# Optimization experiments

Measured on AMD Instinct MI355X. Metric: run time of the kernel, lower is better.

Reference implementation:

```python
import jax, jax.numpy as jnp
import numpy as np
from jax import lax

BLANK = 0


def _rnnt_loss_single(lp, tgt, T_n, U_n):
    """lp: (T, U+1, C) log-probs; tgt: (U,) int32; T_n, U_n: scalar lengths.
    Returns the negative log-likelihood via the alpha forward recursion."""
    T, U1, C = lp.shape
    U = U1 - 1
    blank_lp = lp[:, :, BLANK]                                   # (T, U+1)
    # emit_lp[t, u] = lp[t, u, tgt[u]]
    emit_lp = jnp.take_along_axis(
        lp[:, :U, :], tgt[None, :, None].astype(jnp.int32), axis=2
    )[..., 0]                                                    # (T, U)

    # alpha[0, u] = sum_{v<u} emit_lp[0, v]
    row0 = jnp.concatenate(
        [jnp.zeros((1,), lp.dtype), jnp.cumsum(emit_lp[0])]
    )                                                            # (U+1,)

    def outer(prev_row, xs):
        b_prev, e_row = xs                   # blank_lp[t-1], emit_lp[t]
        c = prev_row + b_prev                # come-from-below (blank) term

        def inner(carry, xs2):
            c_u, e_um1 = xs2
            val = jnp.logaddexp(c_u, carry + e_um1)
            return val, val

        _, rest = lax.scan(inner, c[0], (c[1:], e_row))
        row = jnp.concatenate([c[:1], rest])
        return row, row

    _, rows = lax.scan(outer, row0, (blank_lp[:-1], emit_lp[1:]))
    alpha = jnp.concatenate([row0[None, :], rows], axis=0)       # (T, U+1)

    # log P = alpha[T_n-1, U_n] + log p(blank | T_n-1, U_n)
    ll = alpha[T_n - 1, U_n] + blank_lp[T_n - 1, U_n]
    return -ll


def setup_inputs() -> dict:
    key = jax.random.key(0)
    k1, k2 = jax.random.split(key)
    N, T, U, C = 8, 256, 128, 512
    activations = jax.random.normal(k1, (N, T, U + 1, C), dtype=jnp.float32)
    targets = jax.random.randint(k2, (N, U), 1, C, dtype=jnp.int32)
    activation_lengths = jnp.full((N,), T, dtype=jnp.int32)
    target_lengths = jnp.full((N,), U, dtype=jnp.int32)
    return {
        "activations": activations,
        "targets": targets,
        "activation_lengths": activation_lengths,
        "target_lengths": target_lengths,
    }


def reference(activations, targets, activation_lengths, target_lengths):
    lp = jax.nn.log_softmax(activations, axis=-1)                # (N,T,U+1,C)
    losses = jax.vmap(_rnnt_loss_single)(
        lp, targets, activation_lengths, target_lengths
    )                                                            # (N,)
    return jnp.mean(losses)  # reduction='mean'
```

## Files before the change

### kernel.cpp

```cpp
#include <hip/hip_runtime.h>


#define C_CLASSES 512

__device__ __forceinline__ float wave_max(float v) {
    for (int off = 32; off > 0; off >>= 1)
        v = fmaxf(v, __shfl_xor(v, off, 64));
    return v;
}
__device__ __forceinline__ float wave_sum(float v) {
    for (int off = 32; off > 0; off >>= 1)
        v += __shfl_xor(v, off, 64);
    return v;
}
__device__ __forceinline__ float lae(float a, float b) {
    float m = fmaxf(a, b);
    float t = __expf(-fabsf(a - b));
    return m + __logf(1.0f + t);
}

__global__ __launch_bounds__(256) void k1_lse(
    const float* __restrict__ act, const int* __restrict__ tgt,
    float* __restrict__ blankD, float* __restrict__ emitD,
    int N, int T, int U, int rowsTotal, int dstride, int sampleStride)
{
    const int wave = threadIdx.x >> 6;
    const int lane = threadIdx.x & 63;
    const int r = blockIdx.x * 4 + wave;
    if (r >= rowsTotal) return;

    const int U1 = U + 1;
    const int TU1 = T * U1;
    const int n = r / TU1;
    const int rem = r - n * TU1;
    const int t = rem / U1;
    const int u = rem - t * U1;

    const float4* rp = (const float4*)(act + (size_t)r * C_CLASSES);
    const float4 a = rp[lane];
    const float4 b = rp[64 + lane];

    float m = fmaxf(fmaxf(a.x, a.y), fmaxf(a.z, a.w));
    m = fmaxf(m, fmaxf(fmaxf(b.x, b.y), fmaxf(b.z, b.w)));
    m = wave_max(m);
    float s = __expf(a.x - m) + __expf(a.y - m) + __expf(a.z - m) + __expf(a.w - m)
            + __expf(b.x - m) + __expf(b.y - m) + __expf(b.z - m) + __expf(b.w - m);
    s = wave_sum(s);
    const float lse = m + __logf(s);

    const int d = t + u + 1;
    const size_t base = (size_t)n * sampleStride + (size_t)d * dstride;
    if (lane == 0)
        blankD[base + u] = a.x - lse;
    if (u < U) {
        const int k = tgt[n * U + u];
        const int owner = (k < 256) ? (k >> 2) : ((k - 256) >> 2);
        if (lane == owner) {
            const float4 src = (k < 256) ? a : b;
            const int kk = k & 3;
            const float v = (kk & 2) ? ((kk & 1) ? src.w : src.z)
                                     : ((kk & 1) ? src.y : src.x);
            emitD[base + (u + 1)] = v - lse;
        }
    }
}

__global__ __launch_bounds__(64) void k2_alpha(
    const float* __restrict__ blankD, const float* __restrict__ emitD,
    const int* __restrict__ alen, const int* __restrict__ tlen,
    float* __restrict__ losses, int dstride, int sampleStride)
{
    const int n = blockIdx.x;
    const int l = threadIdx.x;
    const int Tn = alen[n];
    const int Un = tlen[n];
    const int Tn1 = Tn - 1;
    const int Dend = Tn1 + Un;

    const float* __restrict__ bS = blankD + (size_t)n * sampleStride;
    const float* __restrict__ eS = emitD  + (size_t)n * sampleStride;

    const float NEG = -1e30f;
    const int u0 = 2 * l, u1 = 2 * l + 1;

    float p0 = (l == 0) ? 0.0f : NEG;
    float p1 = NEG, p2 = NEG;

    float2 bA, eA, bB, eB;
    float b2A, e2A, b2B, e2B;
#define LDIAG(d, bb, ee, b2, e2)                                   \
    {                                                              \
        const float* brow = bS + (size_t)(d) * dstride;            \
        const float* erow = eS + (size_t)(d) * dstride;            \
        bb = *(const float2*)(brow + u0);                          \
        ee = *(const float2*)(erow + u0);                          \
        b2 = brow[128]; e2 = erow[128];                            \
    }

    LDIAG(1, bA, eA, b2A, e2A);
    LDIAG(2, bB, eB, b2B, e2B);

    for (int d = 1; d <= Dend; ++d) {
        const float2 bb = bA, ee = eA;
        const float b2 = b2A, e2 = e2A;
        bA = bB; eA = eB; b2A = b2B; e2A = e2B;
        int dpf = d + 2; if (dpf > Dend + 1) dpf = Dend + 1;
        LDIAG(dpf, bB, eB, b2B, e2B);

        const float pm1 = __shfl_up(p1, 1, 64);

        const int t0 = d - u0, t1 = d - u1, t2 = d - 128;
        const bool v0 = (t0 >= 0) && (t0 <= Tn1) && (u0 <= Un);
        const bool v1 = (t1 >= 0) && (t1 <= Tn1) && (u1 <= Un);
        const bool v2 = (t2 >= 0) && (t2 <= Tn1) && (128 <= Un);

        const float a0 = (v0 && t0 >= 1) ? p0 + bb.x : NEG;
        const float g0 = (v0 && u0 >= 1) ? pm1 + ee.x : NEG;
        const float a1 = (v1 && t1 >= 1) ? p1 + bb.y : NEG;
        const float g1 = v1 ? p0 + ee.y : NEG;
        const float a2 = (v2 && t2 >= 1) ? p2 + b2 : NEG;
        const float g2 = v2 ? p1 + e2 : NEG;

        const float n0 = lae(a0, g0);
        const float n1 = lae(a1, g1);
        const float n2 = lae(a2, g2);
        p0 = n0; p1 = n1; p2 = n2;
    }
#undef LDIAG

    const float fb = bS[(size_t)(Dend + 1) * dstride + Un];
    if (u0 == Un) losses[n] = -(p0 + fb);
    if (u1 == Un) losses[n] = -(p1 + fb);
    if (l == 63 && Un == 128) losses[n] = -(p2 + fb);
}

__global__ void k3_mean(const float* __restrict__ losses, float* __restrict__ out, int N)
{
    if (threadIdx.x == 0) {
        float s = 0.0f;
        for (int i = 0; i < N; ++i) s += losses[i];
        out[0] = s / (float)N;
    }
}

extern "C" void kernel_launch(void* const* d_in, const int* in_sizes, int n_in,
                              void* d_out, int out_size, void* d_ws, size_t ws_size,
                              hipStream_t stream)
{
    const float* act  = (const float*)d_in[0];
    const int*   tgt  = (const int*)d_in[1];
    const int*   alen = (const int*)d_in[2];
    const int*   tlen = (const int*)d_in[3];

    const int N  = in_sizes[2];
    const int U  = in_sizes[1] / N;
    const int U1 = U + 1;
    const int T  = (int)((long long)in_sizes[0] / ((long long)N * U1 * C_CLASSES));

    const int rows = N * T * U1;
    const int dstride = U1 + 1;
    const int sampleStride = (T + U + 1) * dstride;

    float* ws = (float*)d_ws;
    float* blankD = ws;
    float* emitD  = ws + (size_t)N * sampleStride;
    float* losses = emitD + (size_t)N * sampleStride;

    k1_lse<<<(rows + 3) / 4, 256, 0, stream>>>(act, tgt, blankD, emitD,
                                               N, T, U, rows, dstride, sampleStride);
    k2_alpha<<<N, 64, 0, stream>>>(blankD, emitD, alen, tlen, losses,
                                   dstride, sampleStride);
    k3_mean<<<1, 64, 0, stream>>>(losses, (float*)d_out, N);
}
```

Baseline: 897.3 us.

## Deepen alpha prefetch, use nontemporal loads, fuse mean via atomics

```diff
diff --git a/kernel.cpp b/kernel.cpp
--- a/kernel.cpp
+++ b/kernel.cpp
@@ -2,6 +2,8 @@
 
 
 #define C_CLASSES 512
+
+typedef float v4f __attribute__((ext_vector_type(4)));
 
 __device__ __forceinline__ float wave_max(float v) {
     for (int off = 32; off > 0; off >>= 1)
@@ -22,8 +24,11 @@
 __global__ __launch_bounds__(256) void k1_lse(
     const float* __restrict__ act, const int* __restrict__ tgt,
     float* __restrict__ blankD, float* __restrict__ emitD,
+    float* __restrict__ accum, int* __restrict__ count,
     int N, int T, int U, int rowsTotal, int dstride, int sampleStride)
 {
+    if (blockIdx.x == 0 && threadIdx.x == 0) { accum[0] = 0.0f; count[0] = 0; }
+
     const int wave = threadIdx.x >> 6;
     const int lane = threadIdx.x & 63;
     const int r = blockIdx.x * 4 + wave;
@@ -36,9 +41,9 @@
     const int t = rem / U1;
     const int u = rem - t * U1;
 
-    const float4* rp = (const float4*)(act + (size_t)r * C_CLASSES);
-    const float4 a = rp[lane];
-    const float4 b = rp[64 + lane];
+    const v4f* rp = (const v4f*)(act + (size_t)r * C_CLASSES);
+    const v4f a = __builtin_nontemporal_load(rp + lane);
+    const v4f b = __builtin_nontemporal_load(rp + 64 + lane);
 
     float m = fmaxf(fmaxf(a.x, a.y), fmaxf(a.z, a.w));
     m = fmaxf(m, fmaxf(fmaxf(b.x, b.y), fmaxf(b.z, b.w)));
@@ -56,7 +61,7 @@
         const int k = tgt[n * U + u];
         const int owner = (k < 256) ? (k >> 2) : ((k - 256) >> 2);
         if (lane == owner) {
-            const float4 src = (k < 256) ? a : b;
+            const v4f src = (k < 256) ? a : b;
             const int kk = k & 3;
             const float v = (kk & 2) ? ((kk & 1) ? src.w : src.z)
                                      : ((kk & 1) ? src.y : src.x);
@@ -65,10 +70,12 @@
     }
 }
 
+#define PF 8
 __global__ __launch_bounds__(64) void k2_alpha(
     const float* __restrict__ blankD, const float* __restrict__ emitD,
     const int* __restrict__ alen, const int* __restrict__ tlen,
-    float* __restrict__ losses, int dstride, int sampleStride)
+    float* __restrict__ accum, int* __restrict__ count,
+    float* __restrict__ out, int N, int dstride, int sampleStride)
 {
     const int n = blockIdx.x;
     const int l = threadIdx.x;
@@ -86,8 +93,8 @@
     float p0 = (l == 0) ? 0.0f : NEG;
     float p1 = NEG, p2 = NEG;
 
-    float2 bA, eA, bB, eB;
-    float b2A, e2A, b2B, e2B;
+    float2 bQ[PF], eQ[PF];
+    float b2Q[PF], e2Q[PF];
 #define LDIAG(d, bb, ee, b2, e2)                                   \
     {                                                              \
         const float* brow = bS + (size_t)(d) * dstride;            \
@@ -97,51 +104,62 @@
         b2 = brow[128]; e2 = erow[128];                            \
     }
 
-    LDIAG(1, bA, eA, b2A, e2A);
-    LDIAG(2, bB, eB, b2B, e2B);
+#pragma unroll
+    for (int j = 0; j < PF; ++j) {
+        int dl = 1 + j; if (dl > Dend + 1) dl = Dend + 1;
+        LDIAG(dl, bQ[j], eQ[j], b2Q[j], e2Q[j]);
+    }
 
-    for (int d = 1; d <= Dend; ++d) {
-        const float2 bb = bA, ee = eA;
-        const float b2 = b2A, e2 = e2A;
-        bA = bB; eA = eB; b2A = b2B; e2A = e2B;
-        int dpf = d + 2; if (dpf > Dend + 1) dpf = Dend + 1;
-        LDIAG(dpf, bB, eB, b2B, e2B);
+    for (int d0 = 1; d0 <= Dend; d0 += PF) {
+#pragma unroll
+        for (int j = 0; j < PF; ++j) {
+            const int d = d0 + j;
+            if (d > Dend) break;
 
-        const float pm1 = __shfl_up(p1, 1, 64);
+            const float2 bb = bQ[j], ee = eQ[j];
+            const float b2 = b2Q[j], e2 = e2Q[j];
+            int dpf = d + PF; if (dpf > Dend + 1) dpf = Dend + 1;
+            LDIAG(dpf, bQ[j], eQ[j], b2Q[j], e2Q[j]);
 
-        const int t0 = d - u0, t1 = d - u1, t2 = d - 128;
-        const bool v0 = (t0 >= 0) && (t0 <= Tn1) && (u0 <= Un);
-        const bool v1 = (t1 >= 0) && (t1 <= Tn1) && (u1 <= Un);
-        const bool v2 = (t2 >= 0) && (t2 <= Tn1) && (128 <= Un);
+            const float pm1 = __shfl_up(p1, 1, 64);
 
-        const float a0 = (v0 && t0 >= 1) ? p0 + bb.x : NEG;
-        const float g0 = (v0 && u0 >= 1) ? pm1 + ee.x : NEG;
-        const float a1 = (v1 && t1 >= 1) ? p1 + bb.y : NEG;
-        const float g1 = v1 ? p0 + ee.y : NEG;
-        const float a2 = (v2 && t2 >= 1) ? p2 + b2 : NEG;
-        const float g2 = v2 ? p1 + e2 : NEG;
+            const int t0 = d - u0, t1 = d - u1, t2 = d - 128;
+            const bool v0 = (t0 >= 0) && (t0 <= Tn1) && (u0 <= Un);
+            const bool v1 = (t1 >= 0) && (t1 <= Tn1) && (u1 <= Un);
+            const bool v2 = (t2 >= 0) && (t2 <= Tn1) && (128 <= Un);
 
-        const float n0 = lae(a0, g0);
-        const float n1 = lae(a1, g1);
-        const float n2 = lae(a2, g2);
-        p0 = n0; p1 = n1; p2 = n2;
+            const float a0 = (v0 && t0 >= 1) ? p0 + bb.x : NEG;
+            const float g0 = (v0 && u0 >= 1) ? pm1 + ee.x : NEG;
+            const float a1 = (v1 && t1 >= 1) ? p1 + bb.y : NEG;
+            const float g1 = v1 ? p0 + ee.y : NEG;
+            const float a2 = (v2 && t2 >= 1) ? p2 + b2 : NEG;
+            const float g2 = v2 ? p1 + e2 : NEG;
+
+            p0 = lae(a0, g0);
+            p1 = lae(a1, g1);
+            p2 = lae(a2, g2);
+        }
     }
 #undef LDIAG
 
     const float fb = bS[(size_t)(Dend + 1) * dstride + Un];
-    if (u0 == Un) losses[n] = -(p0 + fb);
-    if (u1 == Un) losses[n] = -(p1 + fb);
-    if (l == 63 && Un == 128) losses[n] = -(p2 + fb);
-}
+    float lv = 0.0f; bool own = false;
+    if (u0 == Un)               { lv = -(p0 + fb); own = true; }
+    if (u1 == Un)               { lv = -(p1 + fb); own = true; }
+    if (l == 63 && Un == 128)   { lv = -(p2 + fb); own = true; }
 
-__global__ void k3_mean(const float* __restrict__ losses, float* __restrict__ out, int N)
-{
-    if (threadIdx.x == 0) {
-        float s = 0.0f;
-        for (int i = 0; i < N; ++i) s += losses[i];
-        out[0] = s / (float)N;
+    if (own) {
+        atomicAdd(accum, lv);
+        __threadfence();
+        const int old = atomicAdd(count, 1);
+        if (old == N - 1) {
+            __threadfence();
+            const float s = atomicAdd(accum, 0.0f);
+            out[0] = s / (float)N;
+        }
     }
 }
+#undef PF
 
 extern "C" void kernel_launch(void* const* d_in, const int* in_sizes, int n_in,
                               void* d_out, int out_size, void* d_ws, size_t ws_size,
@@ -162,13 +180,15 @@
     const int sampleStride = (T + U + 1) * dstride;
 
     float* ws = (float*)d_ws;
-    float* blankD = ws;
-    float* emitD  = ws + (size_t)N * sampleStride;
-    float* losses = emitD + (size_t)N * sampleStride;
+    float* accum  = ws;
+    int*   count  = (int*)(ws + 1);
+    float* blankD = ws + 2;
+    float* emitD  = blankD + (size_t)N * sampleStride;
 
     k1_lse<<<(rows + 3) / 4, 256, 0, stream>>>(act, tgt, blankD, emitD,
+                                               accum, count,
                                                N, T, U, rows, dstride, sampleStride);
-    k2_alpha<<<N, 64, 0, stream>>>(blankD, emitD, alen, tlen, losses,
-                                   dstride, sampleStride);
-    k3_mean<<<1, 64, 0, stream>>>(losses, (float*)d_out, N);
+    k2_alpha<<<N, 64, 0, stream>>>(blankD, emitD, alen, tlen,
+                                   accum, count, (float*)d_out,
+                                   N, dstride, sampleStride);
 }
```

New measurement: 840.0 us. -6.4%, faster.
